# Kernel optimization log

Measured on AMD Instinct MI355X. Metric: run time of the kernel, lower is better.

The kernel has to match this reference:

```python
import jax, jax.numpy as jnp
import numpy as np

B, L, DN, DE, DD, H = 2, 512, 512, 128, 128, 8
DK, DEH, DDH = DN // H, DE // H, DD // H
F = 2 * DK + DEH + 2 * DDH  # per-head concat feature size (176)
SLOPE = 0.2


def _kaiming(key, out_f, in_f):
    bound = np.sqrt(6.0 / ((1.0 + SLOPE ** 2) * in_f))
    return jax.random.uniform(key, (out_f, in_f), minval=-bound, maxval=bound, dtype=jnp.float32)


def lin(x, w, b):
    y = jnp.einsum('...i,oi->...o', x, w)
    return y if b is None else y + b


def setup_inputs() -> dict:
    key = jax.random.key(0)
    ks = jax.random.split(key, 16)
    inp = {
        'node_representation': jax.random.normal(ks[0], (B, L, DN), dtype=jnp.float32),
        'edge_representation': jax.random.normal(ks[1], (B, L, L, DE), dtype=jnp.float32),
        'diff_vec': jax.random.normal(ks[2], (B, L, DD), dtype=jnp.float32),
        'Wn_w': _kaiming(ks[3], DN, DN), 'Wn_b': jnp.zeros((DN,), jnp.float32),
        'We_w': _kaiming(ks[4], DE, DE), 'We_b': jnp.zeros((DE,), jnp.float32),
        'Wd_w': _kaiming(ks[5], DD, DD), 'Wd_b': jnp.zeros((DD,), jnp.float32),
        'Wh_w': _kaiming(ks[6], DK, DK), 'Wh_b': jnp.zeros((DK,), jnp.float32),
        'attn_w': _kaiming(ks[7], 1, F),
        'outn_w': _kaiming(ks[8], DN, DN), 'outn_b': jnp.zeros((DN,), jnp.float32),
        'Wn2_w': _kaiming(ks[9], DN, DN), 'Wn2_b': jnp.zeros((DN,), jnp.float32),
        'We2_w': _kaiming(ks[10], DE, DE), 'We2_b': jnp.zeros((DE,), jnp.float32),
        'Wd2_w': _kaiming(ks[11], DD, DD), 'Wd2_b': jnp.zeros((DD,), jnp.float32),
        'edge_w': _kaiming(ks[12], DEH, F), 'edge_b': jnp.zeros((DEH,), jnp.float32),
        'oute_w': _kaiming(ks[13], DE, DE), 'oute_b': jnp.zeros((DE,), jnp.float32),
    }
    return inp


def reference(node_representation, edge_representation, diff_vec,
              Wn_w, Wn_b, We_w, We_b, Wd_w, Wd_b, Wh_w, Wh_b, attn_w,
              outn_w, outn_b, Wn2_w, Wn2_b, We2_w, We2_b, Wd2_w, Wd2_b,
              edge_w, edge_b, oute_w, oute_b):
    lrelu = lambda x: jax.nn.leaky_relu(x, SLOPE)

    # ---- node update (GAT-style with concat score decomposed per term) ----
    npj = lin(node_representation, Wn_w, Wn_b).reshape(B, L, H, DK)
    epj = lin(edge_representation, We_w, We_b).reshape(B, L, L, H, DEH)
    dpj = lin(diff_vec, Wd_w, Wd_b).reshape(B, L, H, DDH)
    a = attn_w[0]  # concat order: [hi, hj, edge, di, dj]
    a_hi, a_hj = a[:DK], a[DK:2 * DK]
    a_e = a[2 * DK:2 * DK + DEH]
    a_di, a_dj = a[2 * DK + DEH:2 * DK + DEH + DDH], a[-DDH:]
    # scores[b,i,j,h]
    s = (jnp.einsum('blhd,d->blh', npj, a_hi)[:, :, None, :]
         + jnp.einsum('blhd,d->blh', npj, a_hj)[:, None, :, :]
         + jnp.einsum('blmhe,e->blmh', epj, a_e)
         + jnp.einsum('blhd,d->blh', dpj, a_di)[:, :, None, :]
         + jnp.einsum('blhd,d->blh', dpj, a_dj)[:, None, :, :])
    diag = jnp.eye(L, dtype=bool)[None, :, :, None]
    s = jnp.where(diag, -jnp.inf, s)
    probs = jax.nn.softmax(lrelu(s), axis=2)  # softmax over j
    node_wh = lin(npj, Wh_w, Wh_b)  # [B,L,H,DK]
    agg = jnp.einsum('blmh,bmhd->blhd', probs, node_wh)
    new_node = (npj + lrelu(agg)).reshape(B, L, DN)
    new_node = lin(new_node, outn_w, outn_b)

    # ---- edge update (concat-linear decomposed into per-term matmuls) ----
    np2 = lin(new_node, Wn2_w, Wn2_b).reshape(B, L, H, DK)
    ep2 = lin(edge_representation, We2_w, We2_b).reshape(B, L, L, H, DEH)
    dp2 = lin(diff_vec, Wd2_w, Wd2_b).reshape(B, L, H, DDH)
    # edge concat order: [edge, hi, hj, di, dj]
    W_e = edge_w[:, :DEH]
    W_hi = edge_w[:, DEH:DEH + DK]
    W_hj = edge_w[:, DEH + DK:DEH + 2 * DK]
    W_di = edge_w[:, DEH + 2 * DK:DEH + 2 * DK + DDH]
    W_dj = edge_w[:, -DDH:]
    e_out = (jnp.einsum('blmhe,fe->blmhf', ep2, W_e)
             + jnp.einsum('blhd,fd->blhf', np2, W_hi)[:, :, None]
             + jnp.einsum('blhd,fd->blhf', np2, W_hj)[:, None]
             + jnp.einsum('blhd,fd->blhf', dp2, W_di)[:, :, None]
             + jnp.einsum('blhd,fd->blhf', dp2, W_dj)[:, None]
             + edge_b)
    new_edge = lin(e_out.reshape(B, L, L, DE), oute_w, oute_b)
    return new_node, new_edge
```

## Files before the change

kernel.cpp:

```cpp
#include <hip/hip_runtime.h>
#include <hip/hip_bf16.h>

typedef unsigned short u16;
typedef unsigned short u16x8 __attribute__((ext_vector_type(8)));
typedef __bf16 bf16x8 __attribute__((ext_vector_type(8)));
typedef float f32x4 __attribute__((ext_vector_type(4)));

#define LRS 0.2f

__device__ __forceinline__ u16 f2b(float f) {
  __hip_bfloat16 h = __float2bfloat16(f);
  return __builtin_bit_cast(u16, h);
}

template<int K, int O, int KSEG>
__device__ __forceinline__ void gemm_rows4(const float* xr, const float* W, const float* bias,
                                           float* yl, float* yg, int ygstride) {
  constexpr int KPT = K / KSEG;
  constexpr int OPP = 256 / KSEG;
  const int t = threadIdx.x;
  const int ks = t % KSEG;
  const int oi = t / KSEG;
#pragma unroll
  for (int pass = 0; pass < O / OPP; ++pass) {
    const int o = pass * OPP + oi;
    float a0 = 0, a1 = 0, a2 = 0, a3 = 0;
    const float* wp = W + (size_t)o * K + ks * KPT;
    const float* xb = xr + ks * KPT;
#pragma unroll 4
    for (int kc = 0; kc < KPT; kc += 4) {
      f32x4 w4 = *(const f32x4*)(wp + kc);
      const float* xp = xb + kc;
#pragma unroll
      for (int j = 0; j < 4; ++j) {
        float w = w4[j];
        a0 += xp[j] * w;
        a1 += xp[K + j] * w;
        a2 += xp[2 * K + j] * w;
        a3 += xp[3 * K + j] * w;
      }
    }
#pragma unroll
    for (int d = 1; d < KSEG; d <<= 1) {
      a0 += __shfl_xor(a0, d, 64);
      a1 += __shfl_xor(a1, d, 64);
      a2 += __shfl_xor(a2, d, 64);
      a3 += __shfl_xor(a3, d, 64);
    }
    if (ks == 0) {
      float bv = bias ? bias[o] : 0.0f;
      float v0 = a0 + bv, v1 = a1 + bv, v2 = a2 + bv, v3 = a3 + bv;
      if (yl) { yl[o] = v0; yl[O + o] = v1; yl[2 * O + o] = v2; yl[3 * O + o] = v3; }
      if (yg) { yg[o] = v0; yg[ygstride + o] = v1; yg[2 * (size_t)ygstride + o] = v2; yg[3 * (size_t)ygstride + o] = v3; }
    }
  }
}

__global__ __launch_bounds__(256) void kW1(const float* We_w, const float* We_b, const float* attn,
                                           const float* We2_w, const float* We2_b,
                                           const float* edge_w, const float* edge_b,
                                           float* Mfull, float* vf, float* cbe, float* sconst) {
  int gid = blockIdx.x * 256 + threadIdx.x;
  if (gid < 16384) {
    int hf = gid >> 7, c = gid & 127;
    int h = hf >> 4, fo = hf & 15;
    float s = 0;
    for (int e = 0; e < 16; ++e)
      s += edge_w[fo * 176 + e] * We2_w[(h * 16 + e) * 128 + c];
    Mfull[hf * 128 + c] = s;
  } else if (gid < 16384 + 2048) {
    int idx = gid - 16384;
    int c = idx >> 4, hc = idx & 15;
    if (hc < 8) {
      float s = 0;
      for (int e = 0; e < 16; ++e)
        s += We_w[(hc * 16 + e) * 128 + c] * attn[128 + e];
      vf[c * 8 + hc] = s;
    }
  } else if (gid < 18432 + 128) {
    int hf = gid - 18432;
    int h = hf >> 4, fo = hf & 15;
    float s = edge_b[fo];
    for (int e = 0; e < 16; ++e)
      s += We2_b[h * 16 + e] * edge_w[fo * 176 + e];
    cbe[hf] = s;
  } else if (gid < 18560 + 8) {
    int h = gid - 18560;
    float s = 0;
    for (int e = 0; e < 16; ++e)
      s += We_b[h * 16 + e] * attn[128 + e];
    sconst[h] = s;
  }
}

__global__ __launch_bounds__(256) void kW2(const float* oute_w, const float* Mfull, u16* Gb) {
  int gid = blockIdx.x * 256 + threadIdx.x;
  int o = gid >> 7, c = gid & 127;
  float s = 0;
  for (int k = 0; k < 128; ++k)
    s += oute_w[o * 128 + k] * Mfull[k * 128 + c];
  Gb[o * 128 + c] = f2b(s);
}

__global__ __launch_bounds__(256) void kN1(const float* node, const float* diff,
                                           const float* Wn_w, const float* Wn_b,
                                           const float* Wd_w, const float* Wd_b,
                                           const float* Wh_w, const float* Wh_b,
                                           const float* attn, const float* sconst,
                                           float* npj_g, float* nwh_g,
                                           float* srow_g, float* scol_g) {
  __shared__ float nrow[4 * 512], npjl[4 * 512], drow[4 * 128], dpjl[4 * 128];
  const int t = threadIdx.x;
  const int r0 = blockIdx.x * 4;
  *(f32x4*)&nrow[t * 8]     = *(const f32x4*)(node + (size_t)r0 * 512 + t * 8);
  *(f32x4*)&nrow[t * 8 + 4] = *(const f32x4*)(node + (size_t)r0 * 512 + t * 8 + 4);
  if (t < 64) {
    *(f32x4*)&drow[t * 8]     = *(const f32x4*)(diff + (size_t)r0 * 128 + t * 8);
    *(f32x4*)&drow[t * 8 + 4] = *(const f32x4*)(diff + (size_t)r0 * 128 + t * 8 + 4);
  }
  __syncthreads();
  gemm_rows4<512, 512, 4>(nrow, Wn_w, Wn_b, npjl, npj_g + (size_t)r0 * 512, 512);
  gemm_rows4<128, 128, 4>(drow, Wd_w, Wd_b, dpjl, nullptr, 0);
  __syncthreads();
  {
    int d = t & 63, hh = t >> 6;
#pragma unroll
    for (int hi = 0; hi < 2; ++hi) {
      int h = hh + hi * 4;
      float wb = Wh_b[d];
      float acc[4] = {wb, wb, wb, wb};
      for (int k = 0; k < 64; ++k) {
        float w = Wh_w[d * 64 + k];
#pragma unroll
        for (int r = 0; r < 4; ++r) acc[r] += npjl[r * 512 + h * 64 + k] * w;
      }
#pragma unroll
      for (int r = 0; r < 4; ++r) nwh_g[(size_t)(r0 + r) * 512 + h * 64 + d] = acc[r];
    }
  }
  if (t < 32) {
    int r = t >> 3, h = t & 7;
    float shi = 0, shj = 0, sdi = 0, sdj = 0;
    for (int d = 0; d < 64; ++d) {
      float x = npjl[r * 512 + h * 64 + d];
      shi += x * attn[d];
      shj += x * attn[64 + d];
    }
    for (int e = 0; e < 16; ++e) {
      float x = dpjl[r * 128 + h * 16 + e];
      sdi += x * attn[144 + e];
      sdj += x * attn[160 + e];
    }
    srow_g[(r0 + r) * 8 + h] = shi + sdi + sconst[h];
    scol_g[(r0 + r) * 8 + h] = shj + sdj;
  }
}

__global__ __launch_bounds__(256) void kA(const float* edge, const float* npj, const float* nwh,
                                          const float* srow, const float* scol,
                                          const float* vf, float* nnp) {
  __shared__ float s_arr[512][9];
  __shared__ float red[256];
  __shared__ float mxh[8], inv8[8];
  __shared__ float part[2][512];
  const int bl = blockIdx.x;
  const int b = bl >> 9, l = bl & 511;
  const int t = threadIdx.x;

  {
    const int sub = t & 15, rg = t >> 4;
    f32x4 vrx[16];
#pragma unroll
    for (int q = 0; q < 16; ++q) vrx[q] = *(const f32x4*)(vf + sub * 64 + q * 4);
    const float* ebase = edge + (size_t)bl * 65536 + (size_t)rg * 128 + sub * 8;
    f32x4 c0 = *(const f32x4*)ebase;
    f32x4 c1 = *(const f32x4*)(ebase + 4);
    for (int it = 0; it < 32; ++it) {
      f32x4 n0, n1;
      if (it < 31) {
        const float* ep = ebase + (size_t)(it + 1) * 2048;
        n0 = *(const f32x4*)ep;
        n1 = *(const f32x4*)(ep + 4);
      }
      float acc[8];
#pragma unroll
      for (int h2 = 0; h2 < 8; ++h2) acc[h2] = 0.0f;
#pragma unroll
      for (int j = 0; j < 4; ++j) {
#pragma unroll
        for (int h2 = 0; h2 < 8; ++h2) {
          acc[h2] += c0[j] * vrx[j * 2 + (h2 >> 2)][h2 & 3];
          acc[h2] += c1[j] * vrx[8 + j * 2 + (h2 >> 2)][h2 & 3];
        }
      }
#pragma unroll
      for (int d = 1; d < 16; d <<= 1) {
#pragma unroll
        for (int h2 = 0; h2 < 8; ++h2) acc[h2] += __shfl_xor(acc[h2], d, 64);
      }
      if (sub < 8) {
        float a = acc[0];
#pragma unroll
        for (int h2 = 1; h2 < 8; ++h2) if (sub == h2) a = acc[h2];
        s_arr[it * 16 + rg][sub] = a;
      }
      if (it < 31) { c0 = n0; c1 = n1; }
    }
  }
  __syncthreads();

  const int h = t & 7, seg = t >> 3;
  const float srh2 = srow[(size_t)bl * 8 + h];
  float mx = -__builtin_inff();
#pragma unroll 4
  for (int i = 0; i < 16; ++i) {
    int m = seg * 16 + i;
    float sv = s_arr[m][h] + srh2 + scol[((size_t)b * 512 + m) * 8 + h];
    sv = (m == l) ? -__builtin_inff() : (sv >= 0.0f ? sv : LRS * sv);
    s_arr[m][h] = sv;
    mx = fmaxf(mx, sv);
  }
  red[t] = mx;
  __syncthreads();
  if (t < 8) {
    float m2 = -__builtin_inff();
    for (int sg = 0; sg < 32; ++sg) m2 = fmaxf(m2, red[sg * 8 + t]);
    mxh[t] = m2;
  }
  __syncthreads();
  float mh = mxh[h];
  float sm = 0;
#pragma unroll 4
  for (int i = 0; i < 16; ++i) {
    int m = seg * 16 + i;
    float p = __expf(s_arr[m][h] - mh);
    s_arr[m][h] = p;
    sm += p;
  }
  red[t] = sm;
  __syncthreads();
  if (t < 8) {
    float s2 = 0;
    for (int sg = 0; sg < 32; ++sg) s2 += red[sg * 8 + t];
    inv8[t] = 1.0f / s2;
  }
  __syncthreads();

  const int half = t >> 7, oq = t & 127;
  const int o4 = oq * 4, hh = oq >> 4;
  f32x4 acc4a = {0, 0, 0, 0}, acc4b = {0, 0, 0, 0};
  const float* nb = nwh + (size_t)b * 512 * 512;
  for (int m = half * 256; m < half * 256 + 256; m += 2) {
    acc4a += s_arr[m][hh]     * *(const f32x4*)(nb + (size_t)m * 512 + o4);
    acc4b += s_arr[m + 1][hh] * *(const f32x4*)(nb + (size_t)(m + 1) * 512 + o4);
  }
  *(f32x4*)&part[half][o4] = acc4a + acc4b;
  __syncthreads();
  if (t < 128) {
    int ob = t * 4, h2 = t >> 4;
    f32x4 s0 = *(f32x4*)&part[0][ob];
    f32x4 s1 = *(f32x4*)&part[1][ob];
    f32x4 np4 = *(const f32x4*)(npj + (size_t)bl * 512 + ob);
    float iv = inv8[h2];
    f32x4 o;
#pragma unroll
    for (int j = 0; j < 4; ++j) {
      float a = (s0[j] + s1[j]) * iv;
      a = a >= 0.0f ? a : LRS * a;
      o[j] = np4[j] + a;
    }
    *(f32x4*)(nnp + (size_t)bl * 512 + ob) = o;
  }
}

__global__ __launch_bounds__(256) void kN2(const float* nnp, const float* outn_w, const float* outn_b,
                                           float* out0) {
  __shared__ float xr[4 * 512];
  const int t = threadIdx.x;
  const int r0 = blockIdx.x * 4;
  *(f32x4*)&xr[t * 4]        = *(const f32x4*)(nnp + (size_t)r0 * 512 + t * 4);
  *(f32x4*)&xr[1024 + t * 4] = *(const f32x4*)(nnp + (size_t)r0 * 512 + 1024 + t * 4);
  __syncthreads();
  gemm_rows4<512, 512, 4>(xr, outn_w, outn_b, nullptr, out0 + (size_t)r0 * 512, 512);
}

__global__ __launch_bounds__(256) void kN3(const float* nn, const float* diff,
                                           const float* Wn2_w, const float* Wn2_b,
                                           const float* Wd2_w, const float* Wd2_b,
                                           const float* edge_w, const float* cbe,
                                           float* Rl_g, float* Rm_g) {
  __shared__ float xr[4 * 512], np2l[4 * 512], dr[4 * 128], dp2l[4 * 128];
  const int t = threadIdx.x;
  const int r0 = blockIdx.x * 4;
  *(f32x4*)&xr[t * 4]        = *(const f32x4*)(nn + (size_t)r0 * 512 + t * 4);
  *(f32x4*)&xr[1024 + t * 4] = *(const f32x4*)(nn + (size_t)r0 * 512 + 1024 + t * 4);
  if (t < 64) {
    *(f32x4*)&dr[t * 8]     = *(const f32x4*)(diff + (size_t)r0 * 128 + t * 8);
    *(f32x4*)&dr[t * 8 + 4] = *(const f32x4*)(diff + (size_t)r0 * 128 + t * 8 + 4);
  }
  __syncthreads();
  gemm_rows4<512, 512, 4>(xr, Wn2_w, Wn2_b, np2l, nullptr, 0);
  gemm_rows4<128, 128, 4>(dr, Wd2_w, Wd2_b, dp2l, nullptr, 0);
  __syncthreads();
  {
    int hf = t & 127, which = t >> 7;
    int h = hf >> 4, fo = hf & 15;
    const float* wh = edge_w + fo * 176 + 16 + which * 64;
    const float* wd = edge_w + fo * 176 + 144 + which * 16;
    float add = which ? 0.0f : cbe[hf];
    float* dst = which ? Rm_g : Rl_g;
#pragma unroll
    for (int r = 0; r < 4; ++r) {
      float a = add;
      for (int d = 0; d < 64; ++d) a += np2l[r * 512 + h * 64 + d] * wh[d];
      for (int e = 0; e < 16; ++e) a += dp2l[r * 128 + h * 16 + e] * wd[e];
      dst[(size_t)(r0 + r) * 128 + hf] = a;
    }
  }
}

__global__ __launch_bounds__(256) void kN4(const float* Rl, const float* Rm,
                                           const float* oute_w, const float* oute_b,
                                           float* Pl, float* Pm) {
  __shared__ float xl[4 * 128], xm[4 * 128];
  const int t = threadIdx.x;
  const int r0 = blockIdx.x * 4;
  if (t < 128) *(f32x4*)&xl[t * 4] = *(const f32x4*)(Rl + (size_t)r0 * 128 + t * 4);
  else { int q = t - 128; *(f32x4*)&xm[q * 4] = *(const f32x4*)(Rm + (size_t)r0 * 128 + q * 4); }
  __syncthreads();
  gemm_rows4<128, 128, 4>(xl, oute_w, oute_b, nullptr, Pl + (size_t)r0 * 128, 128);
  gemm_rows4<128, 128, 4>(xm, oute_w, nullptr, nullptr, Pm + (size_t)r0 * 128, 128);
}

__global__ __launch_bounds__(256) void kE(const float* edge, const u16* Gb,
                                          const float* Pl, const float* Pm, float* oute) {
  __shared__ u16 Gt[16384];
  __shared__ u16 At[2][8192];
  const int bl = blockIdx.x;
  const int b = bl >> 9;
  const int t = threadIdx.x, lane = t & 63, w = t >> 6;
  const float* Ab = edge + (size_t)bl * 65536;
  const int arow = t >> 2, aseg = t & 3;

  f32x4 pf[8];
  auto issueA = [&](int tile) {
    const float* p = Ab + (size_t)(tile * 64 + arow) * 128 + aseg * 32;
#pragma unroll
    for (int q = 0; q < 8; ++q) pf[q] = *(const f32x4*)(p + q * 4);
  };
  auto writeA = [&](int buf) {
#pragma unroll
    for (int jj = 0; jj < 4; ++jj) {
      u16x8 a8;
#pragma unroll
      for (int j2 = 0; j2 < 4; ++j2) {
        a8[j2]     = f2b(pf[2 * jj][j2]);
        a8[4 + j2] = f2b(pf[2 * jj + 1][j2]);
      }
      int cu = aseg * 4 + jj;
      *(u16x8*)(At[buf] + (arow * 16 + (cu ^ (arow & 7))) * 8) = a8;
    }
  };

  issueA(0);
#pragma unroll
  for (int i2 = 0; i2 < 8; ++i2) {
    int u = i2 * 256 + t;
    int row = u >> 4, cu = u & 15;
    *(u16x8*)(Gt + (row * 16 + (cu ^ (row & 7))) * 8) = *(const u16x8*)(Gb + u * 8);
  }
  writeA(0);
  __syncthreads();

  const int wr = w >> 1, wc = w & 1;
  const int colL = lane & 15, kg = lane >> 4;
  const float* plp = Pl + (size_t)bl * 128;
  float plv[4];
#pragma unroll
  for (int n = 0; n < 4; ++n) plv[n] = plp[wc * 64 + n * 16 + colL];

  for (int tile = 0; tile < 8; ++tile) {
    if (tile < 7) issueA(tile + 1);
    const int buf = tile & 1;
    f32x4 acc[2][4] = {};
#pragma unroll
    for (int ks = 0; ks < 4; ++ks) {
      int cu = ks * 4 + kg;
      bf16x8 af[2], bfv[4];
#pragma unroll
      for (int i = 0; i < 2; ++i) {
        int row = wr * 32 + i * 16 + colL;
        af[i] = *(bf16x8*)(At[buf] + (row * 16 + (cu ^ (row & 7))) * 8);
      }
#pragma unroll
      for (int n = 0; n < 4; ++n) {
        int orow = wc * 64 + n * 16 + colL;
        bfv[n] = *(bf16x8*)(Gt + (orow * 16 + (cu ^ (orow & 7))) * 8);
      }
#pragma unroll
      for (int i = 0; i < 2; ++i)
#pragma unroll
        for (int n = 0; n < 4; ++n)
          acc[i][n] = __builtin_amdgcn_mfma_f32_16x16x32_bf16(af[i], bfv[n], acc[i][n], 0, 0, 0);
    }
    if (tile < 7) writeA(buf ^ 1);
    const int m0 = tile * 64;
    float* ob = oute + ((size_t)bl * 512 + m0) * 128;
#pragma unroll
    for (int i = 0; i < 2; ++i) {
#pragma unroll
      for (int r = 0; r < 4; ++r) {
        int m = wr * 32 + i * 16 + kg * 4 + r;
        const float* pmp = Pm + ((size_t)b * 512 + m0 + m) * 128;
#pragma unroll
        for (int n = 0; n < 4; ++n) {
          int o = wc * 64 + n * 16 + colL;
          ob[(size_t)m * 128 + o] = acc[i][n][r] + plv[n] + pmp[o];
        }
      }
    }
    __syncthreads();
  }
}

extern "C" void kernel_launch(void* const* d_in, const int* in_sizes, int n_in,
                              void* d_out, int out_size, void* d_ws, size_t ws_size,
                              hipStream_t stream) {
  (void)in_sizes; (void)n_in; (void)out_size; (void)ws_size;
  const float* node   = (const float*)d_in[0];
  const float* edge   = (const float*)d_in[1];
  const float* diff   = (const float*)d_in[2];
  const float* Wn_w   = (const float*)d_in[3];
  const float* Wn_b   = (const float*)d_in[4];
  const float* We_w   = (const float*)d_in[5];
  const float* We_b   = (const float*)d_in[6];
  const float* Wd_w   = (const float*)d_in[7];
  const float* Wd_b   = (const float*)d_in[8];
  const float* Wh_w   = (const float*)d_in[9];
  const float* Wh_b   = (const float*)d_in[10];
  const float* attn   = (const float*)d_in[11];
  const float* outn_w = (const float*)d_in[12];
  const float* outn_b = (const float*)d_in[13];
  const float* Wn2_w  = (const float*)d_in[14];
  const float* Wn2_b  = (const float*)d_in[15];
  const float* We2_w  = (const float*)d_in[16];
  const float* We2_b  = (const float*)d_in[17];
  const float* Wd2_w  = (const float*)d_in[18];
  const float* Wd2_b  = (const float*)d_in[19];
  const float* edge_w = (const float*)d_in[20];
  const float* edge_b = (const float*)d_in[21];
  const float* oute_w = (const float*)d_in[22];
  const float* oute_b = (const float*)d_in[23];

  float* out0 = (float*)d_out;
  float* out1 = out0 + 524288;

  float* f = (float*)d_ws;
  size_t off = 0;
  auto alloc = [&](size_t n) { float* p = f + off; off += (n + 7) & ~(size_t)7; return p; };
  float* npj    = alloc(524288);
  float* nwh    = alloc(524288);
  float* srow   = alloc(8192);
  float* scol   = alloc(8192);
  float* sconst = alloc(8);
  float* cbe    = alloc(128);
  float* Mfull  = alloc(16384);
  float* nnp    = alloc(524288);
  float* Rl     = alloc(131072);
  float* Rm     = alloc(131072);
  float* Pl     = alloc(131072);
  float* Pm     = alloc(131072);
  float* vf     = alloc(1024);
  u16* Gb = (u16*)(f + off); off += 8192;

  hipLaunchKernelGGL(kW1, dim3(73), dim3(256), 0, stream,
                     We_w, We_b, attn, We2_w, We2_b, edge_w, edge_b, Mfull, vf, cbe, sconst);
  hipLaunchKernelGGL(kW2, dim3(64), dim3(256), 0, stream, oute_w, Mfull, Gb);
  hipLaunchKernelGGL(kN1, dim3(256), dim3(256), 0, stream,
                     node, diff, Wn_w, Wn_b, Wd_w, Wd_b, Wh_w, Wh_b, attn, sconst,
                     npj, nwh, srow, scol);
  hipLaunchKernelGGL(kA, dim3(1024), dim3(256), 0, stream,
                     edge, npj, nwh, srow, scol, vf, nnp);
  hipLaunchKernelGGL(kN2, dim3(256), dim3(256), 0, stream, nnp, outn_w, outn_b, out0);
  hipLaunchKernelGGL(kN3, dim3(256), dim3(256), 0, stream,
                     out0, diff, Wn2_w, Wn2_b, Wd2_w, Wd2_b, edge_w, cbe, Rl, Rm);
  hipLaunchKernelGGL(kN4, dim3(256), dim3(256), 0, stream, Rl, Rm, oute_w, oute_b, Pl, Pm);
  hipLaunchKernelGGL(kE, dim3(1024), dim3(256), 0, stream, edge, Gb, Pl, Pm, out1);
}
```

Measured before the change: 494.0 us.

## Batch four query rows per attention block, fuse kN3/kN4, split edge kernel grid

The attention kernel now handles four query rows per block, keeping bf16 probabilities in shared memory. This lets one pass over the node_wh matrix serve four rows, cutting its global reads fourfold, but the grid shrinks from 1024 to 256 blocks. kN3 and kN4 are fused so the Rl/Rm intermediates stay in shared memory instead of a global round trip. The edge kernel is split into 4096 smaller blocks without double buffering, and the small GEMM helper uses vectorized x loads. Storing probabilities as bf16 adds precision loss, and the smaller attention grid may reduce occupancy.

```diff
diff --git a/kernel.cpp b/kernel.cpp
--- a/kernel.cpp
+++ b/kernel.cpp
@@ -8,6 +8,7 @@
 
 #define LRS 0.2f
 
+__device__ __forceinline__ float bf2f(u16 u) { return __uint_as_float(((unsigned)u) << 16); }
 __device__ __forceinline__ u16 f2b(float f) {
   __hip_bfloat16 h = __float2bfloat16(f);
   return __builtin_bit_cast(u16, h);
@@ -30,14 +31,17 @@
 #pragma unroll 4
     for (int kc = 0; kc < KPT; kc += 4) {
       f32x4 w4 = *(const f32x4*)(wp + kc);
-      const float* xp = xb + kc;
+      f32x4 x0 = *(const f32x4*)(xb + kc);
+      f32x4 x1 = *(const f32x4*)(xb + K + kc);
+      f32x4 x2 = *(const f32x4*)(xb + 2 * K + kc);
+      f32x4 x3 = *(const f32x4*)(xb + 3 * K + kc);
 #pragma unroll
       for (int j = 0; j < 4; ++j) {
         float w = w4[j];
-        a0 += xp[j] * w;
-        a1 += xp[K + j] * w;
-        a2 += xp[2 * K + j] * w;
-        a3 += xp[3 * K + j] * w;
+        a0 += x0[j] * w;
+        a1 += x1[j] * w;
+        a2 += x2[j] * w;
+        a3 += x3[j] * w;
       }
     }
 #pragma unroll
@@ -159,117 +163,132 @@
 __global__ __launch_bounds__(256) void kA(const float* edge, const float* npj, const float* nwh,
                                           const float* srow, const float* scol,
                                           const float* vf, float* nnp) {
-  __shared__ float s_arr[512][9];
+  __shared__ float sm[4608];
+  __shared__ u16 Pb[4][512][8];
   __shared__ float red[256];
-  __shared__ float mxh[8], inv8[8];
-  __shared__ float part[2][512];
-  const int bl = blockIdx.x;
-  const int b = bl >> 9, l = bl & 511;
+  __shared__ float mxh8[8];
+  __shared__ float inv8v[4][8];
+  const int blk = blockIdx.x;
+  const int b = blk >> 7, lt = blk & 127;
   const int t = threadIdx.x;
-
-  {
-    const int sub = t & 15, rg = t >> 4;
-    f32x4 vrx[16];
-#pragma unroll
-    for (int q = 0; q < 16; ++q) vrx[q] = *(const f32x4*)(vf + sub * 64 + q * 4);
-    const float* ebase = edge + (size_t)bl * 65536 + (size_t)rg * 128 + sub * 8;
-    f32x4 c0 = *(const f32x4*)ebase;
-    f32x4 c1 = *(const f32x4*)(ebase + 4);
-    for (int it = 0; it < 32; ++it) {
-      f32x4 n0, n1;
-      if (it < 31) {
-        const float* ep = ebase + (size_t)(it + 1) * 2048;
-        n0 = *(const f32x4*)ep;
-        n1 = *(const f32x4*)(ep + 4);
-      }
-      float acc[8];
-#pragma unroll
-      for (int h2 = 0; h2 < 8; ++h2) acc[h2] = 0.0f;
-#pragma unroll
-      for (int j = 0; j < 4; ++j) {
-#pragma unroll
-        for (int h2 = 0; h2 < 8; ++h2) {
-          acc[h2] += c0[j] * vrx[j * 2 + (h2 >> 2)][h2 & 3];
-          acc[h2] += c1[j] * vrx[8 + j * 2 + (h2 >> 2)][h2 & 3];
-        }
-      }
-#pragma unroll
-      for (int d = 1; d < 16; d <<= 1) {
-#pragma unroll
-        for (int h2 = 0; h2 < 8; ++h2) acc[h2] += __shfl_xor(acc[h2], d, 64);
-      }
-      if (sub < 8) {
-        float a = acc[0];
-#pragma unroll
-        for (int h2 = 1; h2 < 8; ++h2) if (sub == h2) a = acc[h2];
-        s_arr[it * 16 + rg][sub] = a;
-      }
-      if (it < 31) { c0 = n0; c1 = n1; }
-    }
-  }
-  __syncthreads();
-
+  const int sub = t & 15, rg = t >> 4;
   const int h = t & 7, seg = t >> 3;
-  const float srh2 = srow[(size_t)bl * 8 + h];
-  float mx = -__builtin_inff();
+
+  f32x4 vrx[16];
+#pragma unroll
+  for (int q = 0; q < 16; ++q) vrx[q] = *(const f32x4*)(vf + sub * 64 + q * 4);
+
+  for (int li = 0; li < 4; ++li) {
+    const int l = lt * 4 + li;
+    const size_t bl = (size_t)b * 512 + l;
+    const float* ebase = edge + (bl * 512 + rg) * 128 + sub * 8;
+    f32x4 a0v, a1v, b0v, b1v;
+    a0v = *(const f32x4*)ebase;             a1v = *(const f32x4*)(ebase + 4);
+    b0v = *(const f32x4*)(ebase + 2048);    b1v = *(const f32x4*)(ebase + 2052);
+#define SCORE_ROW(C0, C1, IT)                                                  \
+    {                                                                          \
+      float acc[8];                                                            \
+      _Pragma("unroll") for (int h2 = 0; h2 < 8; ++h2) acc[h2] = 0.0f;         \
+      _Pragma("unroll") for (int j = 0; j < 4; ++j) {                          \
+        _Pragma("unroll") for (int h2 = 0; h2 < 8; ++h2) {                     \
+          acc[h2] += C0[j] * vrx[j * 2 + (h2 >> 2)][h2 & 3];                   \
+          acc[h2] += C1[j] * vrx[8 + j * 2 + (h2 >> 2)][h2 & 3];               \
+        }                                                                      \
+      }                                                                        \
+      _Pragma("unroll") for (int d = 1; d < 16; d <<= 1) {                     \
+        _Pragma("unroll") for (int h2 = 0; h2 < 8; ++h2)                       \
+          acc[h2] += __shfl_xor(acc[h2], d, 64);                               \
+      }                                                                        \
+      if (sub < 8) {                                                           \
+        float a = acc[0];                                                      \
+        _Pragma("unroll") for (int h2 = 1; h2 < 8; ++h2)                       \
+          if (sub == h2) a = acc[h2];                                          \
+        sm[(IT * 16 + rg) * 9 + sub] = a;                                      \
+      }                                                                        \
+    }
+    for (int it = 0; it < 32; it += 2) {
+      SCORE_ROW(a0v, a1v, it);
+      if (it + 2 < 32) {
+        const float* p = ebase + (size_t)(it + 2) * 2048;
+        a0v = *(const f32x4*)p; a1v = *(const f32x4*)(p + 4);
+      }
+      SCORE_ROW(b0v, b1v, (it + 1));
+      if (it + 3 < 32) {
+        const float* p = ebase + (size_t)(it + 3) * 2048;
+        b0v = *(const f32x4*)p; b1v = *(const f32x4*)(p + 4);
+      }
+    }
+#undef SCORE_ROW
+    __syncthreads();
+    const float srh2 = srow[bl * 8 + h];
+    float mx = -__builtin_inff();
 #pragma unroll 4
-  for (int i = 0; i < 16; ++i) {
-    int m = seg * 16 + i;
-    float sv = s_arr[m][h] + srh2 + scol[((size_t)b * 512 + m) * 8 + h];
-    sv = (m == l) ? -__builtin_inff() : (sv >= 0.0f ? sv : LRS * sv);
-    s_arr[m][h] = sv;
-    mx = fmaxf(mx, sv);
-  }
-  red[t] = mx;
-  __syncthreads();
-  if (t < 8) {
-    float m2 = -__builtin_inff();
-    for (int sg = 0; sg < 32; ++sg) m2 = fmaxf(m2, red[sg * 8 + t]);
-    mxh[t] = m2;
-  }
-  __syncthreads();
-  float mh = mxh[h];
-  float sm = 0;
+    for (int i = 0; i < 16; ++i) {
+      int m = seg * 16 + i;
+      float sv = sm[m * 9 + h] + srh2 + scol[((size_t)b * 512 + m) * 8 + h];
+      sv = (m == l) ? -__builtin_inff() : (sv >= 0.0f ? sv : LRS * sv);
+      sm[m * 9 + h] = sv;
+      mx = fmaxf(mx, sv);
+    }
+    red[t] = mx;
+    __syncthreads();
+    if (t < 8) {
+      float m2 = -__builtin_inff();
+      for (int sg = 0; sg < 32; ++sg) m2 = fmaxf(m2, red[sg * 8 + t]);
+      mxh8[t] = m2;
+    }
+    __syncthreads();
+    float mh = mxh8[h];
+    float smv = 0;
 #pragma unroll 4
-  for (int i = 0; i < 16; ++i) {
-    int m = seg * 16 + i;
-    float p = __expf(s_arr[m][h] - mh);
-    s_arr[m][h] = p;
-    sm += p;
-  }
-  red[t] = sm;
-  __syncthreads();
-  if (t < 8) {
-    float s2 = 0;
-    for (int sg = 0; sg < 32; ++sg) s2 += red[sg * 8 + t];
-    inv8[t] = 1.0f / s2;
-  }
-  __syncthreads();
+    for (int i = 0; i < 16; ++i) {
+      int m = seg * 16 + i;
+      float p = __expf(sm[m * 9 + h] - mh);
+      Pb[li][m][h] = f2b(p);
+      smv += p;
+    }
+    red[t] = smv;
+    __syncthreads();
+    if (t < 8) {
+      float s2 = 0;
+      for (int sg = 0; sg < 32; ++sg) s2 += red[sg * 8 + t];
+      inv8v[li][t] = 1.0f / s2;
+    }
+    __syncthreads();
+  }
 
   const int half = t >> 7, oq = t & 127;
   const int o4 = oq * 4, hh = oq >> 4;
-  f32x4 acc4a = {0, 0, 0, 0}, acc4b = {0, 0, 0, 0};
+  f32x4 acc[4] = {};
   const float* nb = nwh + (size_t)b * 512 * 512;
-  for (int m = half * 256; m < half * 256 + 256; m += 2) {
-    acc4a += s_arr[m][hh]     * *(const f32x4*)(nb + (size_t)m * 512 + o4);
-    acc4b += s_arr[m + 1][hh] * *(const f32x4*)(nb + (size_t)(m + 1) * 512 + o4);
-  }
-  *(f32x4*)&part[half][o4] = acc4a + acc4b;
+  for (int m = half * 256; m < half * 256 + 256; ++m) {
+    f32x4 nv = *(const f32x4*)(nb + (size_t)m * 512 + o4);
+#pragma unroll
+    for (int li = 0; li < 4; ++li)
+      acc[li] += bf2f(Pb[li][m][hh]) * nv;
+  }
+#pragma unroll
+  for (int li = 0; li < 4; ++li)
+    *(f32x4*)&sm[(half * 4 + li) * 512 + o4] = acc[li];
   __syncthreads();
   if (t < 128) {
     int ob = t * 4, h2 = t >> 4;
-    f32x4 s0 = *(f32x4*)&part[0][ob];
-    f32x4 s1 = *(f32x4*)&part[1][ob];
-    f32x4 np4 = *(const f32x4*)(npj + (size_t)bl * 512 + ob);
-    float iv = inv8[h2];
-    f32x4 o;
-#pragma unroll
-    for (int j = 0; j < 4; ++j) {
-      float a = (s0[j] + s1[j]) * iv;
-      a = a >= 0.0f ? a : LRS * a;
-      o[j] = np4[j] + a;
-    }
-    *(f32x4*)(nnp + (size_t)bl * 512 + ob) = o;
+#pragma unroll
+    for (int li = 0; li < 4; ++li) {
+      f32x4 s0 = *(f32x4*)&sm[li * 512 + ob];
+      f32x4 s1 = *(f32x4*)&sm[(4 + li) * 512 + ob];
+      const size_t bl = (size_t)b * 512 + lt * 4 + li;
+      f32x4 np4 = *(const f32x4*)(npj + bl * 512 + ob);
+      float iv = inv8v[li][h2];
+      f32x4 o;
+#pragma unroll
+      for (int j = 0; j < 4; ++j) {
+        float a = (s0[j] + s1[j]) * iv;
+        a = a >= 0.0f ? a : LRS * a;
+        o[j] = np4[j] + a;
+      }
+      *(f32x4*)(nnp + bl * 512 + ob) = o;
+    }
   }
 }
 
@@ -284,12 +303,14 @@
   gemm_rows4<512, 512, 4>(xr, outn_w, outn_b, nullptr, out0 + (size_t)r0 * 512, 512);
 }
 
-__global__ __launch_bounds__(256) void kN3(const float* nn, const float* diff,
-                                           const float* Wn2_w, const float* Wn2_b,
-                                           const float* Wd2_w, const float* Wd2_b,
-                                           const float* edge_w, const float* cbe,
-                                           float* Rl_g, float* Rm_g) {
+__global__ __launch_bounds__(256) void kN34(const float* nn, const float* diff,
+                                            const float* Wn2_w, const float* Wn2_b,
+                                            const float* Wd2_w, const float* Wd2_b,
+                                            const float* edge_w, const float* cbe,
+                                            const float* oute_w, const float* oute_b,
+                                            float* Pl, float* Pm) {
   __shared__ float xr[4 * 512], np2l[4 * 512], dr[4 * 128], dp2l[4 * 128];
+  __shared__ float Rls[4 * 128], Rms[4 * 128];
   const int t = threadIdx.x;
   const int r0 = blockIdx.x * 4;
   *(f32x4*)&xr[t * 4]        = *(const f32x4*)(nn + (size_t)r0 * 512 + t * 4);
@@ -308,80 +329,63 @@
     const float* wh = edge_w + fo * 176 + 16 + which * 64;
     const float* wd = edge_w + fo * 176 + 144 + which * 16;
     float add = which ? 0.0f : cbe[hf];
-    float* dst = which ? Rm_g : Rl_g;
+    float* dst = which ? Rms : Rls;
 #pragma unroll
     for (int r = 0; r < 4; ++r) {
       float a = add;
       for (int d = 0; d < 64; ++d) a += np2l[r * 512 + h * 64 + d] * wh[d];
       for (int e = 0; e < 16; ++e) a += dp2l[r * 128 + h * 16 + e] * wd[e];
-      dst[(size_t)(r0 + r) * 128 + hf] = a;
-    }
-  }
-}
-
-__global__ __launch_bounds__(256) void kN4(const float* Rl, const float* Rm,
-                                           const float* oute_w, const float* oute_b,
-                                           float* Pl, float* Pm) {
-  __shared__ float xl[4 * 128], xm[4 * 128];
-  const int t = threadIdx.x;
-  const int r0 = blockIdx.x * 4;
-  if (t < 128) *(f32x4*)&xl[t * 4] = *(const f32x4*)(Rl + (size_t)r0 * 128 + t * 4);
-  else { int q = t - 128; *(f32x4*)&xm[q * 4] = *(const f32x4*)(Rm + (size_t)r0 * 128 + q * 4); }
-  __syncthreads();
-  gemm_rows4<128, 128, 4>(xl, oute_w, oute_b, nullptr, Pl + (size_t)r0 * 128, 128);
-  gemm_rows4<128, 128, 4>(xm, oute_w, nullptr, nullptr, Pm + (size_t)r0 * 128, 128);
+      dst[r * 128 + hf] = a;
+    }
+  }
+  __syncthreads();
+  gemm_rows4<128, 128, 4>(Rls, oute_w, oute_b, nullptr, Pl + (size_t)r0 * 128, 128);
+  gemm_rows4<128, 128, 4>(Rms, oute_w, nullptr, nullptr, Pm + (size_t)r0 * 128, 128);
 }
 
 __global__ __launch_bounds__(256) void kE(const float* edge, const u16* Gb,
                                           const float* Pl, const float* Pm, float* oute) {
   __shared__ u16 Gt[16384];
-  __shared__ u16 At[2][8192];
-  const int bl = blockIdx.x;
+  __shared__ u16 At[8192];
+  const int tile = blockIdx.x;
+  const int bl = tile >> 2;
   const int b = bl >> 9;
+  const int q0 = (tile & 3) * 128;
   const int t = threadIdx.x, lane = t & 63, w = t >> 6;
-  const float* Ab = edge + (size_t)bl * 65536;
-  const int arow = t >> 2, aseg = t & 3;
-
-  f32x4 pf[8];
-  auto issueA = [&](int tile) {
-    const float* p = Ab + (size_t)(tile * 64 + arow) * 128 + aseg * 32;
-#pragma unroll
-    for (int q = 0; q < 8; ++q) pf[q] = *(const f32x4*)(p + q * 4);
-  };
-  auto writeA = [&](int buf) {
-#pragma unroll
-    for (int jj = 0; jj < 4; ++jj) {
-      u16x8 a8;
-#pragma unroll
-      for (int j2 = 0; j2 < 4; ++j2) {
-        a8[j2]     = f2b(pf[2 * jj][j2]);
-        a8[4 + j2] = f2b(pf[2 * jj + 1][j2]);
-      }
-      int cu = aseg * 4 + jj;
-      *(u16x8*)(At[buf] + (arow * 16 + (cu ^ (arow & 7))) * 8) = a8;
-    }
-  };
-
-  issueA(0);
 #pragma unroll
   for (int i2 = 0; i2 < 8; ++i2) {
     int u = i2 * 256 + t;
     int row = u >> 4, cu = u & 15;
     *(u16x8*)(Gt + (row * 16 + (cu ^ (row & 7))) * 8) = *(const u16x8*)(Gb + u * 8);
   }
-  writeA(0);
-  __syncthreads();
-
   const int wr = w >> 1, wc = w & 1;
   const int colL = lane & 15, kg = lane >> 4;
   const float* plp = Pl + (size_t)bl * 128;
   float plv[4];
 #pragma unroll
   for (int n = 0; n < 4; ++n) plv[n] = plp[wc * 64 + n * 16 + colL];
-
-  for (int tile = 0; tile < 8; ++tile) {
-    if (tile < 7) issueA(tile + 1);
-    const int buf = tile & 1;
+  const int arow = t >> 2, aseg = t & 3;
+
+  for (int sub = 0; sub < 2; ++sub) {
+    const int r0 = q0 + sub * 64;
+    {
+      const float* p = edge + ((size_t)bl * 512 + r0 + arow) * 128 + aseg * 32;
+      f32x4 v[8];
+#pragma unroll
+      for (int q = 0; q < 8; ++q) v[q] = *(const f32x4*)(p + q * 4);
+#pragma unroll
+      for (int jj = 0; jj < 4; ++jj) {
+        u16x8 a8;
+#pragma unroll
+        for (int j2 = 0; j2 < 4; ++j2) {
+          a8[j2]     = f2b(v[2 * jj][j2]);
+          a8[4 + j2] = f2b(v[2 * jj + 1][j2]);
+        }
+        int cu = aseg * 4 + jj;
+        *(u16x8*)(At + (arow * 16 + (cu ^ (arow & 7))) * 8) = a8;
+      }
+    }
+    __syncthreads();
     f32x4 acc[2][4] = {};
 #pragma unroll
     for (int ks = 0; ks < 4; ++ks) {
@@ -390,7 +394,7 @@
 #pragma unroll
       for (int i = 0; i < 2; ++i) {
         int row = wr * 32 + i * 16 + colL;
-        af[i] = *(bf16x8*)(At[buf] + (row * 16 + (cu ^ (row & 7))) * 8);
+        af[i] = *(bf16x8*)(At + (row * 16 + (cu ^ (row & 7))) * 8);
       }
 #pragma unroll
       for (int n = 0; n < 4; ++n) {
@@ -403,15 +407,13 @@
         for (int n = 0; n < 4; ++n)
           acc[i][n] = __builtin_amdgcn_mfma_f32_16x16x32_bf16(af[i], bfv[n], acc[i][n], 0, 0, 0);
     }
-    if (tile < 7) writeA(buf ^ 1);
-    const int m0 = tile * 64;
-    float* ob = oute + ((size_t)bl * 512 + m0) * 128;
+    float* ob = oute + ((size_t)bl * 512 + r0) * 128;
 #pragma unroll
     for (int i = 0; i < 2; ++i) {
 #pragma unroll
       for (int r = 0; r < 4; ++r) {
         int m = wr * 32 + i * 16 + kg * 4 + r;
-        const float* pmp = Pm + ((size_t)b * 512 + m0 + m) * 128;
+        const float* pmp = Pm + ((size_t)b * 512 + r0 + m) * 128;
 #pragma unroll
         for (int n = 0; n < 4; ++n) {
           int o = wc * 64 + n * 16 + colL;
@@ -466,8 +468,6 @@
   float* cbe    = alloc(128);
   float* Mfull  = alloc(16384);
   float* nnp    = alloc(524288);
-  float* Rl     = alloc(131072);
-  float* Rm     = alloc(131072);
   float* Pl     = alloc(131072);
   float* Pm     = alloc(131072);
   float* vf     = alloc(1024);
@@ -479,11 +479,10 @@
   hipLaunchKernelGGL(kN1, dim3(256), dim3(256), 0, stream,
                      node, diff, Wn_w, Wn_b, Wd_w, Wd_b, Wh_w, Wh_b, attn, sconst,
                      npj, nwh, srow, scol);
-  hipLaunchKernelGGL(kA, dim3(1024), dim3(256), 0, stream,
+  hipLaunchKernelGGL(kA, dim3(256), dim3(256), 0, stream,
                      edge, npj, nwh, srow, scol, vf, nnp);
   hipLaunchKernelGGL(kN2, dim3(256), dim3(256), 0, stream, nnp, outn_w, outn_b, out0);
-  hipLaunchKernelGGL(kN3, dim3(256), dim3(256), 0, stream,
-                     out0, diff, Wn2_w, Wn2_b, Wd2_w, Wd2_b, edge_w, cbe, Rl, Rm);
-  hipLaunchKernelGGL(kN4, dim3(256), dim3(256), 0, stream, Rl, Rm, oute_w, oute_b, Pl, Pm);
-  hipLaunchKernelGGL(kE, dim3(1024), dim3(256), 0, stream, edge, Gb, Pl, Pm, out1);
-}
+  hipLaunchKernelGGL(kN34, dim3(256), dim3(256), 0, stream,
+                     out0, diff, Wn2_w, Wn2_b, Wd2_w, Wd2_b, edge_w, cbe, oute_w, oute_b, Pl, Pm);
+  hipLaunchKernelGGL(kE, dim3(4096), dim3(256), 0, stream, edge, Gb, Pl, Pm, out1);
+}
```

Result: faster. 472.7 us (-4.3%).
